# Performance work log

Hardware: AMD Instinct MI355X
Metric: run time of the kernel (lower is better)

## Reference

```python
import jax, jax.numpy as jnp
import numpy as np

B, S, D, H, DFF = 2, 2048, 1024, 16, 4096
DK = D // H
EPS = 1e-6


def setup_inputs() -> dict:
    key = jax.random.key(0)
    ks = jax.random.split(key, 16)
    s = lambda fan_in: 1.0 / np.sqrt(fan_in)
    inp = {
        "xb": jax.random.normal(ks[0], (B, S, D), jnp.float32),
        "mask": jnp.ones((B, 1, 1, S), jnp.int32),
        "Wq": jax.random.normal(ks[1], (D, D), jnp.float32) * s(D),
        "bq": jnp.zeros((D,), jnp.float32),
        "Wk": jax.random.normal(ks[2], (D, D), jnp.float32) * s(D),
        "bk": jnp.zeros((D,), jnp.float32),
        "Wv": jax.random.normal(ks[3], (D, D), jnp.float32) * s(D),
        "bv": jnp.zeros((D,), jnp.float32),
        "Wo": jax.random.normal(ks[4], (D, D), jnp.float32) * s(D),
        "bo": jnp.zeros((D,), jnp.float32),
        "W1": jax.random.normal(ks[5], (D, DFF), jnp.float32) * s(D),
        "b1": jnp.zeros((DFF,), jnp.float32),
        "W2": jax.random.normal(ks[6], (DFF, D), jnp.float32) * s(DFF),
        "b2": jnp.zeros((D,), jnp.float32),
        "a1": jnp.ones((1,), jnp.float32),
        "o1": jnp.zeros((1,), jnp.float32),
        "a2": jnp.ones((1,), jnp.float32),
        "o2": jnp.zeros((1,), jnp.float32),
    }
    return inp


def layernorm(x, alpha, bias):
    # matches LayerNormalization: unbiased std (torch default), scalar alpha/bias,
    # division by (std + eps)
    mean = jnp.mean(x, axis=-1, keepdims=True)
    var = jnp.sum((x - mean) ** 2, axis=-1, keepdims=True) / (x.shape[-1] - 1)
    std = jnp.sqrt(var)
    return alpha * (x - mean) / (std + EPS) + bias


def mha(x, mask, Wq, bq, Wk, bk, Wv, bv, Wo, bo):
    b, s, d = x.shape
    q = (x @ Wq + bq).reshape(b, s, H, DK).transpose(0, 2, 1, 3)  # [B,H,S,DK]
    k = (x @ Wk + bk).reshape(b, s, H, DK).transpose(0, 2, 1, 3)
    v = (x @ Wv + bv).reshape(b, s, H, DK).transpose(0, 2, 1, 3)
    logits = jnp.einsum("bhqd,bhkd->bhqk", q, k) / np.sqrt(DK)
    logits = jnp.where(mask == 0, jnp.float32(-1e9), logits)
    probs = jax.nn.softmax(logits, axis=-1)
    a = jnp.einsum("bhqk,bhkd->bhqd", probs, v)  # [B,H,S,DK]
    a = a.transpose(0, 2, 1, 3).reshape(b, s, d)
    return a @ Wo + bo


def reference(xb, mask, Wq, bq, Wk, bk, Wv, bv, Wo, bo, W1, b1, W2, b2, a1, o1, a2, o2):
    # residual 1: x + MHA(LN(x))  (dropout disabled: eval mode)
    h = xb + mha(layernorm(xb, a1, o1), mask, Wq, bq, Wk, bk, Wv, bv, Wo, bo)
    # residual 2: h + FFN(LN(h))
    z = layernorm(h, a2, o2)
    ff = jax.nn.relu(z @ W1 + b1) @ W2 + b2
    return h + ff
```

## Files before the change

### kernel.cpp

```cpp
#include <hip/hip_runtime.h>
#include <hip/hip_bf16.h>
#include <math.h>

typedef __bf16 bf16x8 __attribute__((ext_vector_type(8)));
typedef float f32x4 __attribute__((ext_vector_type(4)));
typedef float f32x16 __attribute__((ext_vector_type(16)));
typedef unsigned short u16;

#define DEV __device__ __forceinline__

static constexpr int Bc = 2, Sc = 2048, Dc = 1024, Hc = 16, DFFc = 4096, DKc = 64;
static constexpr int Mc = Bc * Sc;
static constexpr float QSCALE = 0.125f * 1.4426950408889634f;

DEV u16 f32_to_bf16(float x) {
    unsigned u = __builtin_bit_cast(unsigned, x);
    u += 0x7FFFu + ((u >> 16) & 1u);
    return (u16)(u >> 16);
}

DEV float bf16_to_f32(u16 h) {
    return __builtin_bit_cast(float, (unsigned)h << 16);
}

DEV float exp2_fast(float x) {
    float r;
    asm("v_exp_f32 %0, %1" : "=v"(r) : "v"(x));
    return r;
}

DEV unsigned cvt_pk_bf16(float lo, float hi_) {
    unsigned r;
    asm("v_cvt_pk_bf16_f32 %0, %1, %2" : "=v"(r) : "v"(lo), "v"(hi_));
    return r;
}

DEV void gload_lds16(const u16* g, u16* l) {
    __builtin_amdgcn_global_load_lds(
        (const __attribute__((address_space(1))) void*)g,
        (__attribute__((address_space(3))) void*)l, 16, 0, 0);
}

DEV float block_reduce_sum(float v) {
    __shared__ float part[4];
    int lane = threadIdx.x & 63, w = threadIdx.x >> 6;
    #pragma unroll
    for (int m = 1; m < 64; m <<= 1) v += __shfl_xor(v, m);
    __syncthreads();
    if (lane == 0) part[w] = v;
    __syncthreads();
    return part[0] + part[1] + part[2] + part[3];
}

__global__ __launch_bounds__(256)
void ln_kernel(const float* __restrict__ x, u16* __restrict__ y,
               const float* __restrict__ alpha, const float* __restrict__ beta) {
    long row = blockIdx.x;
    const float4 v = reinterpret_cast<const float4*>(x + row * Dc)[threadIdx.x];
    float s = v.x + v.y + v.z + v.w;
    s = block_reduce_sum(s);
    float mean = s * (1.0f / Dc);
    float d0 = v.x - mean, d1 = v.y - mean, d2 = v.z - mean, d3 = v.w - mean;
    float ss = d0*d0 + d1*d1 + d2*d2 + d3*d3;
    ss = block_reduce_sum(ss);
    float stdv = sqrtf(ss / (float)(Dc - 1));
    float sc = alpha[0] / (stdv + 1e-6f);
    float bi = beta[0];
    ushort4 o;
    o.x = f32_to_bf16(d0 * sc + bi);
    o.y = f32_to_bf16(d1 * sc + bi);
    o.z = f32_to_bf16(d2 * sc + bi);
    o.w = f32_to_bf16(d3 * sc + bi);
    reinterpret_cast<ushort4*>(y + row * Dc)[threadIdx.x] = o;
}

__global__ void transpose_all_kernel(const float* __restrict__ Wq, const float* __restrict__ Wk,
                                     const float* __restrict__ Wv, const float* __restrict__ Wo,
                                     const float* __restrict__ W1, const float* __restrict__ W2,
                                     u16* __restrict__ out) {
    __shared__ float tile[32][33];
    const int id = blockIdx.x;
    const float* in; u16* o; int N, t;
    if (id < 4096) {
        const int w = id >> 10; t = id & 1023;
        in = w == 0 ? Wq : w == 1 ? Wk : w == 2 ? Wv : Wo;
        o = out + (size_t)w * 1024 * 1024;
        N = 1024;
    } else if (id < 8192) {
        t = id - 4096; in = W1; o = out + (size_t)4 * 1024 * 1024; N = 4096;
    } else {
        t = id - 8192; in = W2; o = out + (size_t)8 * 1024 * 1024; N = 1024;
    }
    const int ntx = N >> 5;
    const int n0 = (t % ntx) * 32, k0 = (t / ntx) * 32;
    const int K = (id >= 8192) ? 4096 : 1024;
    const int tx = threadIdx.x, ty = threadIdx.y;
    #pragma unroll
    for (int i = 0; i < 4; i++)
        tile[ty + i*8][tx] = in[(long)(k0 + ty + i*8) * N + n0 + tx];
    __syncthreads();
    #pragma unroll
    for (int i = 0; i < 4; i++)
        o[(long)(n0 + ty + i*8) * K + k0 + tx] = f32_to_bf16(tile[tx][ty + i*8]);
}

enum { EPI_QKV = 0, EPI_RELU = 1, EPI_RES = 2 };

template<int EPI, int BM, int BN, bool DB>
__global__ __launch_bounds__(256, 3)
void gemm_kernel(const u16* __restrict__ A, const u16* __restrict__ BT,
                 const float* __restrict__ b0, const float* __restrict__ b1,
                 const float* __restrict__ b2, void* __restrict__ outp,
                 const float* __restrict__ res, int M, int N, int K) {
    constexpr int BK = 64, RI = BM / 32, RJ = BN / 32;
    constexpr int NB = DB ? 2 : 1;
    __shared__ u16 As[NB][BM * BK];
    __shared__ u16 Bs[NB][BN * BK];
    const int tid = threadIdx.x;
    const int wave = tid >> 6, lane = tid & 63;
    const int wr = wave >> 1, wc = wave & 1;
    const int lr = lane & 15, lg = lane >> 4;
    const int m0 = blockIdx.y * BM, n0 = blockIdx.x * BN;
    const int z = blockIdx.z;
    const u16* Bz = (EPI == EPI_QKV) ? BT + (size_t)z * N * K : BT;

    const int srow = lane >> 3;
    const int scol = ((lane & 7) ^ srow) * 8;

    f32x4 acc[RI][RJ] = {};

    const u16* ap[RI];
    const u16* bp[RJ];
    #pragma unroll
    for (int i = 0; i < RI; i++) ap[i] = A  + (size_t)(m0 + (wave*RI + i)*8 + srow) * K + scol;
    #pragma unroll
    for (int j = 0; j < RJ; j++) bp[j] = Bz + (size_t)(n0 + (wave*RJ + j)*8 + srow) * K + scol;

    auto stage = [&](int bi, int kt) {
        #pragma unroll
        for (int i = 0; i < RI; i++) gload_lds16(ap[i] + kt, &As[bi][(wave*RI + i) * 512]);
        #pragma unroll
        for (int j = 0; j < RJ; j++) gload_lds16(bp[j] + kt, &Bs[bi][(wave*RJ + j) * 512]);
    };
    auto compute = [&](int bi) {
        #pragma unroll
        for (int ks = 0; ks < BK; ks += 32) {
            const int u = (((ks >> 3) + lg) ^ (lr & 7)) * 8;
            bf16x8 a[RI], b[RJ];
            #pragma unroll
            for (int i = 0; i < RI; i++)
                a[i] = *reinterpret_cast<const bf16x8*>(&As[bi][(wr*(BM/2) + i*16 + lr) * BK + u]);
            #pragma unroll
            for (int j = 0; j < RJ; j++)
                b[j] = *reinterpret_cast<const bf16x8*>(&Bs[bi][(wc*(BN/2) + j*16 + lr) * BK + u]);
            #pragma unroll
            for (int i = 0; i < RI; i++)
                #pragma unroll
                for (int j = 0; j < RJ; j++)
                    acc[i][j] = __builtin_amdgcn_mfma_f32_16x16x32_bf16(a[i], b[j], acc[i][j], 0, 0, 0);
        }
    };

    if constexpr (DB) {
        const int nT = K / BK;
        stage(0, 0);
        __syncthreads();
        for (int t = 0; t < nT; t++) {
            const int cur = t & 1;
            if (t + 1 < nT) stage(cur ^ 1, (t + 1) * BK);
            compute(cur);
            __syncthreads();
        }
    } else {
        for (int kt = 0; kt < K; kt += BK) {
            stage(0, kt);
            __syncthreads();
            compute(0);
            __syncthreads();
        }
    }

    const float* bias = (EPI == EPI_QKV) ? (z == 0 ? b0 : z == 1 ? b1 : b2) : b0;
    #pragma unroll
    for (int i = 0; i < RI; i++) {
        #pragma unroll
        for (int j = 0; j < RJ; j++) {
            const int col = n0 + wc*(BN/2) + j*16 + lr;
            const float bv = bias[col];
            #pragma unroll
            for (int rg = 0; rg < 4; rg++) {
                const int row = m0 + wr*(BM/2) + i*16 + lg*4 + rg;
                float val = acc[i][j][rg] + bv;
                if constexpr (EPI == EPI_QKV) {
                    int bb = row >> 11, s = row & (Sc - 1);
                    int hh = col >> 6, dk = col & 63;
                    u16* o = (u16*)outp + (size_t)z * Mc * Dc;
                    if (z == 2)
                        o[((size_t)(bb * Hc + hh) * DKc + dk) * Sc + s] = f32_to_bf16(val);
                    else
                        o[(((size_t)(bb * Hc + hh) * Sc + s) << 6) + dk] =
                            f32_to_bf16(z == 0 ? val * QSCALE : val);
                } else if constexpr (EPI == EPI_RELU) {
                    ((u16*)outp)[(size_t)row * N + col] = f32_to_bf16(fmaxf(val, 0.0f));
                } else {
                    size_t idx = (size_t)row * N + col;
                    ((float*)outp)[idx] = res[idx] + val;
                }
            }
        }
    }
}

__global__ __launch_bounds__(256, 4)
void attn_kernel(const u16* __restrict__ Qg, const u16* __restrict__ Kg,
                 const u16* __restrict__ VTg, const int* __restrict__ mask,
                 u16* __restrict__ part, float* __restrict__ lsum) {
    constexpr int KVB = 64, NT = (Sc / 2) / KVB;
    __shared__ u16 Ks[2][KVB * DKc];
    __shared__ u16 VTs[2][KVB * DKc];
    __shared__ float mbs[Sc / 2];
    __shared__ int wflag[4];

    const int tid = threadIdx.x;
    const int wave = tid >> 6, lane = tid & 63;
    const int l31 = lane & 31, hi = lane >> 5;
    const int bh = blockIdx.y, b = bh >> 4, hh = bh & 15;
    const int q0 = blockIdx.x * 128 + wave * 32;
    const int z = blockIdx.z, kv0 = z * (Sc / 2);
    const long base = (long)bh * Sc * DKc;

    {
        const int4 mv = *reinterpret_cast<const int4*>(&mask[b * Sc + kv0 + tid * 4]);
        float4 f;
        f.x = mv.x ? 0.f : -1e9f;
        f.y = mv.y ? 0.f : -1e9f;
        f.z = mv.z ? 0.f : -1e9f;
        f.w = mv.w ? 0.f : -1e9f;
        *reinterpret_cast<float4*>(&mbs[tid * 4]) = f;
        const bool ok = mv.x && mv.y && mv.z && mv.w;
        const unsigned long long bad = __ballot(!ok);
        if (lane == 0) wflag[wave] = (bad != 0ULL);
    }

    bf16x8 qf[4];
    {
        const u16* qrow = Qg + base + (long)(q0 + l31) * DKc + hi * 8;
        #pragma unroll
        for (int s = 0; s < 4; s++)
            qf[s] = *reinterpret_cast<const bf16x8*>(qrow + s * 16);
    }

    const int unit0 = wave * 128 + lane;
    const int r0 = unit0 >> 3, u0 = unit0 & 7;
    const int c8 = (u0 ^ (r0 & 7)) * 8;
    const u16* ksrc = Kg  + base + (size_t)(kv0 + r0) * DKc + c8;
    const u16* vsrc = VTg + base + (size_t)r0 * Sc + kv0 + c8;

    auto stage = [&](int bi, int kt) {
        gload_lds16(ksrc + (size_t)kt * DKc,       &Ks [bi][wave * 1024]);
        gload_lds16(ksrc + (size_t)(kt + 8) * DKc, &Ks [bi][wave * 1024 + 512]);
        gload_lds16(vsrc + kt,                     &VTs[bi][wave * 1024]);
        gload_lds16(vsrc + kt + 8 * Sc,            &VTs[bi][wave * 1024 + 512]);
    };

    stage(0, 0);
    __syncthreads();

    const bool anyMasked = (wflag[0] | wflag[1] | wflag[2] | wflag[3]) != 0;

    f32x16 accO[2] = {};
    float lrun = 0.f;

    for (int t = 0; t < NT; t++) {
        const int cur = t & 1;
        if (t + 1 < NT) stage(cur ^ 1, (t + 1) * KVB);

        f32x16 st[2];
        #pragma unroll
        for (int kt2 = 0; kt2 < 2; kt2++) {
            f32x16 s = {};
            const int row = kt2 * 32 + l31;
            #pragma unroll
            for (int step = 0; step < 4; step++) {
                const int unit = (step * 2 + hi) ^ (row & 7);
                bf16x8 kf = *reinterpret_cast<const bf16x8*>(&Ks[cur][row * DKc + unit * 8]);
                s = __builtin_amdgcn_mfma_f32_32x32x16_bf16(kf, qf[step], s, 0, 0, 0);
            }
            st[kt2] = s;
        }

        if (anyMasked) {
            #pragma unroll
            for (int kt2 = 0; kt2 < 2; kt2++) {
                #pragma unroll
                for (int g = 0; g < 4; g++) {
                    const float4 mb = *reinterpret_cast<const float4*>(
                        &mbs[t * KVB + kt2 * 32 + g * 8 + hi * 4]);
                    st[kt2][g*4+0] += mb.x;
                    st[kt2][g*4+1] += mb.y;
                    st[kt2][g*4+2] += mb.z;
                    st[kt2][g*4+3] += mb.w;
                }
            }
        }

        float rs0 = 0.f, rs1 = 0.f, rs2 = 0.f, rs3 = 0.f;
        #pragma unroll
        for (int kt2 = 0; kt2 < 2; kt2++) {
            #pragma unroll
            for (int r = 0; r < 16; r += 4) {
                const float p0 = exp2_fast(st[kt2][r+0]);
                const float p1 = exp2_fast(st[kt2][r+1]);
                const float p2 = exp2_fast(st[kt2][r+2]);
                const float p3 = exp2_fast(st[kt2][r+3]);
                st[kt2][r+0] = p0; rs0 += p0;
                st[kt2][r+1] = p1; rs1 += p1;
                st[kt2][r+2] = p2; rs2 += p2;
                st[kt2][r+3] = p3; rs3 += p3;
            }
        }
        lrun += (rs0 + rs1) + (rs2 + rs3);

        #pragma unroll
        for (int kt2 = 0; kt2 < 2; kt2++) {
            #pragma unroll
            for (int kstep = 0; kstep < 2; kstep++) {
                unsigned w0 = cvt_pk_bf16(st[kt2][kstep*8+0], st[kt2][kstep*8+1]);
                unsigned w1 = cvt_pk_bf16(st[kt2][kstep*8+2], st[kt2][kstep*8+3]);
                unsigned w2 = cvt_pk_bf16(st[kt2][kstep*8+4], st[kt2][kstep*8+5]);
                unsigned w3 = cvt_pk_bf16(st[kt2][kstep*8+6], st[kt2][kstep*8+7]);
                const unsigned p0 = (unsigned)__shfl_xor((int)w0, 32);
                const unsigned p1 = (unsigned)__shfl_xor((int)w1, 32);
                const unsigned p2 = (unsigned)__shfl_xor((int)w2, 32);
                const unsigned p3 = (unsigned)__shfl_xor((int)w3, 32);
                uint4 e;
                e.x = hi ? p2 : w0;
                e.y = hi ? p3 : w1;
                e.z = hi ? w2 : p0;
                e.w = hi ? w3 : p1;
                const bf16x8 pa = __builtin_bit_cast(bf16x8, e);
                #pragma unroll
                for (int dt = 0; dt < 2; dt++) {
                    const int drow = dt * 32 + l31;
                    const int unit = (kt2 * 4 + kstep * 2 + hi) ^ (drow & 7);
                    bf16x8 vf = *reinterpret_cast<const bf16x8*>(&VTs[cur][drow * DKc + unit * 8]);
                    accO[dt] = __builtin_amdgcn_mfma_f32_32x32x16_bf16(pa, vf, accO[dt], 0, 0, 0);
                }
            }
        }
        __syncthreads();
    }

    lrun += __shfl_xor(lrun, 32);

    u16* pz = part + (size_t)z * Mc * Dc;
    #pragma unroll
    for (int r = 0; r < 16; r++) {
        const int qr = (r & 3) + 8 * (r >> 2) + 4 * hi;
        u16* po = pz + ((long)(b * Sc + q0 + qr)) * Dc + hh * 64;
        po[l31]      = f32_to_bf16(accO[0][r]);
        po[32 + l31] = f32_to_bf16(accO[1][r]);
    }
    if (hi == 0)
        lsum[((size_t)z * Bc * Hc + bh) * Sc + q0 + l31] = lrun;
}

__global__ __launch_bounds__(256)
void combine_kernel(const u16* __restrict__ part, const float* __restrict__ lsum,
                    u16* __restrict__ Aout) {
    const int idx = blockIdx.x * 256 + threadIdx.x;
    const int row = idx >> 7, g = idx & 127, d0 = g * 8;
    const int b = row >> 11, s = row & (Sc - 1), hh = d0 >> 6;
    const int bh = b * Hc + hh;
    const float l0 = lsum[(size_t)bh * Sc + s];
    const float l1 = lsum[((size_t)Bc * Hc + bh) * Sc + s];
    const float rinv = 1.0f / (l0 + l1);
    const uint4 pa = *reinterpret_cast<const uint4*>(part + (size_t)row * Dc + d0);
    const uint4 pb = *reinterpret_cast<const uint4*>(part + (size_t)Mc * Dc + (size_t)row * Dc + d0);
    const u16* ha = (const u16*)&pa;
    const u16* hb = (const u16*)&pb;
    ushort4 o[2];
    #pragma unroll
    for (int h = 0; h < 2; h++) {
        #pragma unroll
        for (int e = 0; e < 4; e++) {
            float v = (bf16_to_f32(ha[h*4+e]) + bf16_to_f32(hb[h*4+e])) * rinv;
            (&o[h].x)[e] = f32_to_bf16(v);
        }
    }
    *reinterpret_cast<ushort4*>(Aout + (size_t)row * Dc + d0)     = o[0];
    *reinterpret_cast<ushort4*>(Aout + (size_t)row * Dc + d0 + 4) = o[1];
}

extern "C" void kernel_launch(void* const* d_in, const int* in_sizes, int n_in,
                              void* d_out, int out_size, void* d_ws, size_t ws_size,
                              hipStream_t stream) {
    (void)in_sizes; (void)n_in; (void)out_size; (void)ws_size;
    const float* xb = (const float*)d_in[0];
    const int*  mask = (const int*)d_in[1];
    const float* Wq = (const float*)d_in[2];
    const float* bq = (const float*)d_in[3];
    const float* Wk = (const float*)d_in[4];
    const float* bk = (const float*)d_in[5];
    const float* Wv = (const float*)d_in[6];
    const float* bv = (const float*)d_in[7];
    const float* Wo = (const float*)d_in[8];
    const float* bo = (const float*)d_in[9];
    const float* W1 = (const float*)d_in[10];
    const float* b1 = (const float*)d_in[11];
    const float* W2 = (const float*)d_in[12];
    const float* b2 = (const float*)d_in[13];
    const float* a1 = (const float*)d_in[14];
    const float* o1 = (const float*)d_in[15];
    const float* a2 = (const float*)d_in[16];
    const float* o2 = (const float*)d_in[17];
    float* out = (float*)d_out;

    char* p = (char*)d_ws;
    auto alloc = [&](size_t bytes) { char* r = p; p += (bytes + 255) & ~(size_t)255; return r; };
    u16* xln   = (u16*)alloc((size_t)Mc * Dc * 2);
    u16* WTqkv = (u16*)alloc((size_t)3 * Dc * Dc * 2);
    u16* WTo   = (u16*)alloc((size_t)Dc * Dc * 2);
    u16* WT1   = (u16*)alloc((size_t)Dc * DFFc * 2);
    u16* WT2   = (u16*)alloc((size_t)DFFc * Dc * 2);
    u16* qkv   = (u16*)alloc((size_t)3 * Mc * Dc * 2);
    u16* Aat   = (u16*)alloc((size_t)Mc * Dc * 2);
    float* hbuf = (float*)alloc((size_t)Mc * Dc * 4);
    u16* zb  = (u16*)alloc((size_t)Mc * Dc * 2);
    u16* ffh = (u16*)alloc((size_t)Mc * DFFc * 2);
    (void)WTo; (void)WT1;

    u16*   apart = (u16*)ffh;
    float* alsum = (float*)hbuf;

    transpose_all_kernel<<<12288, dim3(32, 8), 0, stream>>>(Wq, Wk, Wv, Wo, W1, W2, WTqkv);

    ln_kernel<<<Mc, 256, 0, stream>>>(xb, xln, a1, o1);

    gemm_kernel<EPI_QKV, 128, 128, false><<<dim3(Dc/128, Mc/128, 3), 256, 0, stream>>>(
        xln, WTqkv, bq, bk, bv, qkv, nullptr, Mc, Dc, Dc);

    attn_kernel<<<dim3(Sc/128, Bc*Hc, 2), 256, 0, stream>>>(
        qkv, qkv + (size_t)Mc*Dc, qkv + (size_t)2*Mc*Dc, mask, apart, alsum);

    combine_kernel<<<(Mc * Dc / 8) / 256, 256, 0, stream>>>(apart, alsum, Aat);

    gemm_kernel<EPI_RES, 128, 64, true><<<dim3(Dc/64, Mc/128), 256, 0, stream>>>(
        Aat, WTo, bo, nullptr, nullptr, hbuf, xb, Mc, Dc, Dc);

    ln_kernel<<<Mc, 256, 0, stream>>>(hbuf, zb, a2, o2);

    gemm_kernel<EPI_RELU, 128, 128, false><<<dim3(DFFc/128, Mc/128), 256, 0, stream>>>(
        zb, WT1, b1, nullptr, nullptr, ffh, nullptr, Mc, DFFc, Dc);

    gemm_kernel<EPI_RES, 128, 64, true><<<dim3(Dc/64, Mc/128), 256, 0, stream>>>(
        ffh, WT2, b2, nullptr, nullptr, out, hbuf, Mc, Dc, DFFc);
}
```

Before: 231.1 us.

## Add 8-wave 256x128 triple-buffered GEMM for QKV and FFN1

```diff
diff --git a/kernel.cpp b/kernel.cpp
--- a/kernel.cpp
+++ b/kernel.cpp
@@ -205,6 +205,132 @@
                 } else {
                     size_t idx = (size_t)row * N + col;
                     ((float*)outp)[idx] = res[idx] + val;
+                }
+            }
+        }
+    }
+}
+
+enum { EPI8_QKVF = 0, EPI8_RELU = 1 };
+
+template<int EPI>
+__global__ __launch_bounds__(512, 2)
+void gemm8p_kernel(const u16* __restrict__ A, const u16* __restrict__ BT,
+                   const float* __restrict__ b0, const float* __restrict__ b1,
+                   const float* __restrict__ b2, u16* __restrict__ outp,
+                   int M, int N, int K) {
+    constexpr int BM = 256, BN = 128, BK = 64;
+    __shared__ u16 As[3][BM * BK];
+    __shared__ u16 Bs[3][BN * BK];
+    const int tid = threadIdx.x;
+    const int wave = tid >> 6, lane = tid & 63;
+    const int wm = wave >> 2, wn = wave & 3;
+    const int lr = lane & 15, lg = lane >> 4;
+    const int m0 = blockIdx.y * BM, n0 = blockIdx.x * BN;
+
+    const int srow = lane >> 3;
+    const int scol = ((lane & 7) ^ srow) * 8;
+    const u16* Ap = A  + (size_t)(m0 + 8*wave + srow) * K + scol;
+    const u16* Bp = BT + (size_t)(n0 + 8*wave + srow) * K + scol;
+
+    auto stage_unit = [&](int slot, int kt, int u) {
+        if (u < 4)
+            gload_lds16(Ap + (size_t)(64*u) * K + kt, &As[slot][(64*u + 8*wave) * BK]);
+        else
+            gload_lds16(Bp + (size_t)(64*(u-4)) * K + kt, &Bs[slot][(64*(u-4) + 8*wave) * BK]);
+    };
+
+    f32x4 acc[8][2] = {};
+    const int nT = K / BK;
+
+    #pragma unroll
+    for (int u = 0; u < 6; u++) stage_unit(0, 0, u);
+    #pragma unroll
+    for (int u = 0; u < 6; u++) stage_unit(1, BK, u);
+
+    for (int t = 0; t < nT; t++) {
+        const int slot = t % 3;
+        const u16* as = As[slot];
+        const u16* bs = Bs[slot];
+
+        if (t < nT - 1) asm volatile("s_waitcnt vmcnt(6)" ::: "memory");
+        else            asm volatile("s_waitcnt vmcnt(0)" ::: "memory");
+        __builtin_amdgcn_sched_barrier(0);
+        __builtin_amdgcn_s_barrier();
+        __builtin_amdgcn_sched_barrier(0);
+
+        #pragma unroll
+        for (int ph = 0; ph < 2; ph++) {
+            bf16x8 af[4][2], bf[2][2];
+            #pragma unroll
+            for (int i = 0; i < 4; i++)
+                #pragma unroll
+                for (int ks = 0; ks < 2; ks++) {
+                    const int row = wm*128 + (ph*4 + i)*16 + lr;
+                    const int u = ((ks*4 + lg) ^ (lr & 7)) * 8;
+                    af[i][ks] = *reinterpret_cast<const bf16x8*>(&as[row * BK + u]);
+                }
+            #pragma unroll
+            for (int j = 0; j < 2; j++)
+                #pragma unroll
+                for (int ks = 0; ks < 2; ks++) {
+                    const int row = wn*32 + j*16 + lr;
+                    const int u = ((ks*4 + lg) ^ (lr & 7)) * 8;
+                    bf[j][ks] = *reinterpret_cast<const bf16x8*>(&bs[row * BK + u]);
+                }
+            if (t + 2 < nT) {
+                const int s2 = (t + 2) % 3, k2 = (t + 2) * BK;
+                stage_unit(s2, k2, ph*3 + 0);
+                stage_unit(s2, k2, ph*3 + 1);
+                stage_unit(s2, k2, ph*3 + 2);
+            }
+            asm volatile("s_waitcnt lgkmcnt(8)" ::: "memory");
+            __builtin_amdgcn_s_barrier();
+            asm volatile("s_waitcnt lgkmcnt(0)" ::: "memory");
+            __builtin_amdgcn_sched_barrier(0);
+            __builtin_amdgcn_s_setprio(1);
+            #pragma unroll
+            for (int i = 0; i < 4; i++)
+                #pragma unroll
+                for (int j = 0; j < 2; j++) {
+                    acc[ph*4+i][j] = __builtin_amdgcn_mfma_f32_16x16x32_bf16(
+                        af[i][0], bf[j][0], acc[ph*4+i][j], 0, 0, 0);
+                    acc[ph*4+i][j] = __builtin_amdgcn_mfma_f32_16x16x32_bf16(
+                        af[i][1], bf[j][1], acc[ph*4+i][j], 0, 0, 0);
+                }
+            __builtin_amdgcn_s_setprio(0);
+            __builtin_amdgcn_sched_barrier(0);
+            __builtin_amdgcn_s_barrier();
+        }
+    }
+
+    #pragma unroll
+    for (int i = 0; i < 8; i++) {
+        #pragma unroll
+        for (int j = 0; j < 2; j++) {
+            const int col = n0 + wn*32 + j*16 + lr;
+            if constexpr (EPI == EPI8_QKVF) {
+                const int zsel = col >> 10, c = col & 1023;
+                const float bv = (zsel == 0 ? b0 : zsel == 1 ? b1 : b2)[c];
+                const int hh = c >> 6, dk = c & 63;
+                u16* o = outp + (size_t)zsel * Mc * Dc;
+                #pragma unroll
+                for (int rg = 0; rg < 4; rg++) {
+                    const int row = m0 + wm*128 + i*16 + lg*4 + rg;
+                    const int bb = row >> 11, s = row & (Sc - 1);
+                    const float val = acc[i][j][rg] + bv;
+                    if (zsel == 2)
+                        o[((size_t)(bb * Hc + hh) * DKc + dk) * Sc + s] = f32_to_bf16(val);
+                    else
+                        o[(((size_t)(bb * Hc + hh) * Sc + s) << 6) + dk] =
+                            f32_to_bf16(zsel == 0 ? val * QSCALE : val);
+                }
+            } else {
+                const float bv = b0[col];
+                #pragma unroll
+                for (int rg = 0; rg < 4; rg++) {
+                    const int row = m0 + wm*128 + i*16 + lg*4 + rg;
+                    outp[(size_t)row * N + col] = f32_to_bf16(fmaxf(acc[i][j][rg] + bv, 0.0f));
                 }
             }
         }
@@ -437,8 +563,8 @@
 
     ln_kernel<<<Mc, 256, 0, stream>>>(xb, xln, a1, o1);
 
-    gemm_kernel<EPI_QKV, 128, 128, false><<<dim3(Dc/128, Mc/128, 3), 256, 0, stream>>>(
-        xln, WTqkv, bq, bk, bv, qkv, nullptr, Mc, Dc, Dc);
+    gemm8p_kernel<EPI8_QKVF><<<dim3(3 * Dc / 128, Mc / 256), 512, 0, stream>>>(
+        xln, WTqkv, bq, bk, bv, qkv, Mc, 3 * Dc, Dc);
 
     attn_kernel<<<dim3(Sc/128, Bc*Hc, 2), 256, 0, stream>>>(
         qkv, qkv + (size_t)Mc*Dc, qkv + (size_t)2*Mc*Dc, mask, apart, alsum);
@@ -450,8 +576,8 @@
 
     ln_kernel<<<Mc, 256, 0, stream>>>(hbuf, zb, a2, o2);
 
-    gemm_kernel<EPI_RELU, 128, 128, false><<<dim3(DFFc/128, Mc/128), 256, 0, stream>>>(
-        zb, WT1, b1, nullptr, nullptr, ffh, nullptr, Mc, DFFc, Dc);
+    gemm8p_kernel<EPI8_RELU><<<dim3(DFFc / 128, Mc / 256), 512, 0, stream>>>(
+        zb, WT1, b1, nullptr, nullptr, ffh, Mc, DFFc, Dc);
 
     gemm_kernel<EPI_RES, 128, 64, true><<<dim3(Dc/64, Mc/128), 256, 0, stream>>>(
         ffh, WT2, b2, nullptr, nullptr, out, hbuf, Mc, Dc, DFFc);
```

Measured after the change: 260.0 us. 12.5% more time.
